# Kernel optimization log

Hardware: AMD Instinct MI355X
Metric: run time of the kernel (lower is better)

## Reference

```python
import jax, jax.numpy as jnp
import numpy as np

BATCH, T, N_STATES, EMIT = 128, 8192, 128, 64


def setup_inputs() -> dict:
    key = jax.random.key(0)
    kobs, kI, kA, kB = jax.random.split(key, 4)
    # one-hot observation sequences, as fed to the RNN cell
    obs = jax.random.randint(kobs, (BATCH, T), 0, EMIT)
    inputs = jax.nn.one_hot(obs, EMIT, dtype=jnp.float32)  # [B, T, EMIT]
    # valid probability parameters (model.I/A/B produce normalized matrices)
    I = jax.nn.softmax(jax.random.normal(kI, (N_STATES,), dtype=jnp.float32))
    A = jax.nn.softmax(jax.random.normal(kA, (N_STATES, N_STATES), dtype=jnp.float32), axis=-1)
    B = jax.nn.softmax(jax.random.normal(kB, (EMIT, N_STATES), dtype=jnp.float32), axis=0)
    return {"inputs": inputs, "I": I, "A": A, "B": B}


def reference(inputs, I, A, B):
    # HMM scaled forward algorithm, exactly the CgpHmmCell.call math,
    # run over the sequence with lax.scan (what keras.layers.RNN does step-wise).
    x = jnp.swapaxes(inputs, 0, 1)  # [T, batch, EMIT]

    # t == 0 (count == 1): R = I, Z = 1
    E0 = x[0] @ B                               # [batch, S]
    alpha0 = E0 * I[None, :]                    # [batch, S]
    loglik0 = jnp.log(jnp.sum(alpha0, axis=-1, keepdims=True))  # [batch, 1]

    def step(carry, x_t):
        alpha, loglik = carry
        Z = jnp.sum(alpha, axis=-1, keepdims=True)      # Z_{i-1}
        R = (alpha / Z) @ A                             # scaled forward @ A
        E = x_t @ B                                     # emission probs
        alpha_new = E * R
        loglik_new = loglik + jnp.log(jnp.sum(alpha_new, axis=-1, keepdims=True))
        return (alpha_new, loglik_new), None

    (alpha_f, loglik_f), _ = jax.lax.scan(step, (alpha0, loglik0), x[1:])
    return alpha_f, loglik_f
```

## Files before the change

kernel.cpp:

```cpp
#include <hip/hip_runtime.h>


#define BATCH 128
#define TLEN 8192
#define NS 128
#define EMIT 64
#define NCHUNK 256
#define CLEN (TLEN / NCHUNK)
#define WARM 8
#define BG 8
#define BSTR 132
#define LN64 4.158883083359672f

typedef __attribute__((ext_vector_type(8))) short short8;
typedef __attribute__((ext_vector_type(4))) float floatx4;
typedef __attribute__((ext_vector_type(4))) unsigned int uintx4;

__device__ __forceinline__ unsigned f2bf(float f) {
    return (__float_as_uint(f) + 0x8000u) >> 16;
}

__global__ __launch_bounds__(256) void decode_onehot(
        const floatx4* __restrict__ x, unsigned char* __restrict__ obsG,
        float* __restrict__ out_ll) {
    if (blockIdx.x == 0 && threadIdx.x < BATCH) out_ll[threadIdx.x] = 0.f;
    int base = blockIdx.x * 512 + threadIdx.x;
    #pragma unroll
    for (int h = 0; h < 2; ++h) {
        int i = base + h * 256;
        floatx4 v = __builtin_nontemporal_load(&x[i]);
        float s = v.x + v.y + v.z + v.w;
        if (s > 0.5f) {
            int e = (v.y > 0.5f) ? 1 : (v.z > 0.5f) ? 2 : (v.w > 0.5f) ? 3 : 0;
            int elem = (i << 2) + e;
            int row = elem >> 6;
            int col = elem & 63;
            int b = row >> 13;
            int t = row & (TLEN - 1);
            obsG[(b >> 4) * (16 * TLEN) + (b & 15) * TLEN + t] = (unsigned char)col;
        }
    }
}

__global__ __launch_bounds__(64) void hmm_scan(
        const float* __restrict__ Amat,
        const float* __restrict__ Bmat,
        const float* __restrict__ Ivec,
        const unsigned char* __restrict__ obsG,
        float* __restrict__ out_alpha,
        float* __restrict__ out_ll)
{
    __shared__ unsigned short Bl[EMIT * BSTR];

    const int lane = threadIdx.x;
    const int n = lane & 15;
    const int q = lane >> 4;
    const int bg = blockIdx.x >> 8;
    const int c = blockIdx.x & (NCHUNK - 1);
    const bool first = (c == 0);
    const bool lastc = (c == NCHUNK - 1);
    const int steps = first ? CLEN : (CLEN + WARM);
    const int t0 = first ? 0 : c * CLEN - WARM;

    for (int i = lane; i < EMIT * NS; i += 64) {
        int e = i >> 7, col = i & (NS - 1);
        Bl[e * BSTR + col] = (unsigned short)f2bf(64.0f * Bmat[i]);
    }

    const unsigned char* orow = obsG + bg * (16 * TLEN) + n * TLEN;
    unsigned ow[10];
    if (first) {
        uintx4 a = *(const uintx4*)(orow);
        uintx4 b = *(const uintx4*)(orow + 16);
        ow[0] = a.x; ow[1] = a.y; ow[2] = a.z; ow[3] = a.w;
        ow[4] = b.x; ow[5] = b.y; ow[6] = b.z; ow[7] = b.w;
        ow[8] = 0; ow[9] = 0;
    } else {
        uint2 a = *(const uint2*)(orow + t0);
        uintx4 b = *(const uintx4*)(orow + t0 + 8);
        uintx4 d = *(const uintx4*)(orow + t0 + 24);
        ow[0] = a.x; ow[1] = a.y;
        ow[2] = b.x; ow[3] = b.y; ow[4] = b.z; ow[5] = b.w;
        ow[6] = d.x; ow[7] = d.y; ow[8] = d.z; ow[9] = d.w;
    }

    short8 af[8][4];
    #pragma unroll
    for (int mt = 0; mt < 8; ++mt)
        #pragma unroll
        for (int kf = 0; kf < 4; ++kf) {
            short8 v;
            #pragma unroll
            for (int j = 0; j < 8; ++j) {
                int u = 32 * kf + 8 * q + j;
                int sk = 32 * (u >> 5) + 16 * ((u >> 2) & 1)
                       + 4 * ((u >> 3) & 3) + (u & 3);
                v[j] = (short)f2bf(Amat[sk * NS + 16 * mt + n]);
            }
            af[mt][kf] = v;
        }
    __syncthreads();

    unsigned pk[16];
    #pragma unroll
    for (int i = 0; i < 16; ++i) pk[i] = 0x3C003C00u;

    float s_pre = 1.0f, s_penult = 1.0f, s_end = 1.0f;

    for (int it = 0; it < steps; ++it) {
        floatx4 acc[8];
        if (first && it == 0) {
            #pragma unroll
            for (int mt = 0; mt < 8; ++mt)
                acc[mt] = *(const floatx4*)(Ivec + 16 * mt + 4 * q);
        } else {
            short8 bf[4];
            #pragma unroll
            for (int kf = 0; kf < 4; ++kf) {
                uintx4 u4 = {pk[4 * kf], pk[4 * kf + 1], pk[4 * kf + 2], pk[4 * kf + 3]};
                bf[kf] = __builtin_bit_cast(short8, u4);
            }
            #pragma unroll
            for (int mt = 0; mt < 8; ++mt) {
                floatx4 a = {0.f, 0.f, 0.f, 0.f};
                #pragma unroll
                for (int kf = 0; kf < 4; ++kf)
                    a = __builtin_amdgcn_mfma_f32_16x16x32_bf16(af[mt][kf], bf[kf], a, 0, 0, 0);
                acc[mt] = a;
            }
        }

        int o = (ow[it >> 2] >> ((it & 3) * 8)) & 0xFF;
        int eb = o * BSTR;
        #pragma unroll
        for (int mt = 0; mt < 8; ++mt) {
            const unsigned* ep = (const unsigned*)(Bl + eb + 16 * mt + 4 * q);
            unsigned d0 = ep[0], d1 = ep[1];
            acc[mt].x *= __uint_as_float(d0 << 16);
            acc[mt].y *= __uint_as_float(d0 & 0xFFFF0000u);
            acc[mt].z *= __uint_as_float(d1 << 16);
            acc[mt].w *= __uint_as_float(d1 & 0xFFFF0000u);
        }

        bool need_red = (it == steps - 1) || (!first && it == WARM - 1) ||
                        (lastc && it == steps - 2);
        if (need_red) {
            float zz = 0.f;
            #pragma unroll
            for (int mt = 0; mt < 8; ++mt)
                zz += (acc[mt].x + acc[mt].y) + (acc[mt].z + acc[mt].w);
            zz += __shfl_xor(zz, 16, 64);
            zz += __shfl_xor(zz, 32, 64);
            if (it == steps - 1) s_end = zz;
            else if (lastc && it == steps - 2) s_penult = zz;
            else s_pre = zz;
        }

        if (lastc && it == steps - 1) {
            float inv = 1.0f / (64.0f * s_penult);
            #pragma unroll
            for (int mt = 0; mt < 8; ++mt) {
                floatx4 o4;
                o4.x = acc[mt].x * inv; o4.y = acc[mt].y * inv;
                o4.z = acc[mt].z * inv; o4.w = acc[mt].w * inv;
                *(floatx4*)(out_alpha + (bg * 16 + n) * NS + 16 * mt + 4 * q) = o4;
            }
        }

        #pragma unroll
        for (int mt = 0; mt < 8; ++mt) {
            unsigned u0 = __float_as_uint(acc[mt].x) + 0x8000u;
            unsigned u1 = __float_as_uint(acc[mt].y) + 0x8000u;
            unsigned u2 = __float_as_uint(acc[mt].z) + 0x8000u;
            unsigned u3 = __float_as_uint(acc[mt].w) + 0x8000u;
            pk[2 * mt]     = __builtin_amdgcn_perm(u1, u0, 0x07060302u);
            pk[2 * mt + 1] = __builtin_amdgcn_perm(u3, u2, 0x07060302u);
        }
    }

    if (q == 0) {
        float ll = __logf(s_end) - __logf(s_pre) - (float)CLEN * LN64;
        atomicAdd(&out_ll[bg * 16 + n], ll);
    }
}

extern "C" void kernel_launch(void* const* d_in, const int* in_sizes, int n_in,
                              void* d_out, int out_size, void* d_ws, size_t ws_size,
                              hipStream_t stream) {
    const float* x = (const float*)d_in[0];
    const float* I = (const float*)d_in[1];
    const float* A = (const float*)d_in[2];
    const float* B = (const float*)d_in[3];
    float* out = (float*)d_out;

    unsigned char* obsG = (unsigned char*)d_ws;

    decode_onehot<<<(BATCH * TLEN * 16) / 512, 256, 0, stream>>>(
        (const floatx4*)x, obsG, out + BATCH * NS);
    hmm_scan<<<BG * NCHUNK, 64, 0, stream>>>(A, B, I, obsG, out, out + BATCH * NS);
}
```

Before: 388.8 us.

## Fuse one-hot decoding into the HMM scan kernel with pipelined prefetch

Removes the separate decode kernel and its byte-index workspace. The scan kernel now streams the one-hot input rows itself, issuing nontemporal loads two steps ahead and decoding each step's observations through a small double-buffered LDS array while the MFMA recurrence runs. It also raises wave priority around the MFMA block, adds an occupancy hint to the launch bounds, and zeroes the log-likelihood output with a memset. The aim is to hide the one-hot input traffic behind the latency-bound serial recurrence. The risks are that the warm-up overlap makes each block re-read part of the input and that each step now waits on more memory latency.

```diff
diff --git a/kernel.cpp b/kernel.cpp
--- a/kernel.cpp
+++ b/kernel.cpp
@@ -20,37 +20,116 @@
     return (__float_as_uint(f) + 0x8000u) >> 16;
 }
 
-__global__ __launch_bounds__(256) void decode_onehot(
-        const floatx4* __restrict__ x, unsigned char* __restrict__ obsG,
-        float* __restrict__ out_ll) {
-    if (blockIdx.x == 0 && threadIdx.x < BATCH) out_ll[threadIdx.x] = 0.f;
-    int base = blockIdx.x * 512 + threadIdx.x;
-    #pragma unroll
-    for (int h = 0; h < 2; ++h) {
-        int i = base + h * 256;
-        floatx4 v = __builtin_nontemporal_load(&x[i]);
-        float s = v.x + v.y + v.z + v.w;
-        if (s > 0.5f) {
-            int e = (v.y > 0.5f) ? 1 : (v.z > 0.5f) ? 2 : (v.w > 0.5f) ? 3 : 0;
-            int elem = (i << 2) + e;
-            int row = elem >> 6;
-            int col = elem & 63;
-            int b = row >> 13;
-            int t = row & (TLEN - 1);
-            obsG[(b >> 4) * (16 * TLEN) + (b & 15) * TLEN + t] = (unsigned char)col;
-        }
-    }
-}
-
-__global__ __launch_bounds__(64) void hmm_scan(
+
+#define ISSUE(P0, P1, P2, P3, s) do {                                     \
+    int _o = (s) * 16;                                                    \
+    P0 = __builtin_nontemporal_load(&X[b0 + _o]);                         \
+    P1 = __builtin_nontemporal_load(&X[b1 + _o]);                         \
+    P2 = __builtin_nontemporal_load(&X[b2 + _o]);                         \
+    P3 = __builtin_nontemporal_load(&X[b3 + _o]);                         \
+} while (0)
+
+#define DEC1(V, g, par) do {                                              \
+    float _s = V.x + V.y + V.z + V.w;                                     \
+    if (_s > 0.5f) {                                                      \
+        int _e = (dcol << 2) +                                            \
+                 ((V.y > 0.5f) ? 1 : (V.z > 0.5f) ? 2 :                   \
+                  (V.w > 0.5f) ? 3 : 0);                                  \
+        obsb[par][4 * (g) + drow] = (unsigned char)_e;                    \
+    }                                                                     \
+} while (0)
+
+#define DECODE(P0, P1, P2, P3, par, dst) do {                             \
+    DEC1(P0, 0, par); DEC1(P1, 1, par);                                   \
+    DEC1(P2, 2, par); DEC1(P3, 3, par);                                   \
+    dst = obsb[par][n];                                                   \
+} while (0)
+
+#define STEP(IT, RA0, RA1, RA2, RA3, RB0, RB1, RB2, RB3, PAR) do {        \
+    int _nx = (IT) + 2; if (_nx > steps - 1) _nx = steps - 1;             \
+    ISSUE(RA0, RA1, RA2, RA3, _nx);                                       \
+    int _onx = o_cur;                                                     \
+    if ((IT) + 1 < steps) DECODE(RB0, RB1, RB2, RB3, PAR, _onx);          \
+    floatx4 acc[8];                                                       \
+    if (first && (IT) == 0) {                                             \
+        _Pragma("unroll")                                                 \
+        for (int mt = 0; mt < 8; ++mt)                                    \
+            acc[mt] = *(const floatx4*)(Ivec + 16 * mt + 4 * q);          \
+    } else {                                                              \
+        short8 bf[4];                                                     \
+        _Pragma("unroll")                                                 \
+        for (int kf = 0; kf < 4; ++kf) {                                  \
+            uintx4 _u4 = {pk[4 * kf], pk[4 * kf + 1],                     \
+                          pk[4 * kf + 2], pk[4 * kf + 3]};                \
+            bf[kf] = __builtin_bit_cast(short8, _u4);                     \
+        }                                                                 \
+        __builtin_amdgcn_s_setprio(1);                                    \
+        _Pragma("unroll")                                                 \
+        for (int mt = 0; mt < 8; ++mt) {                                  \
+            floatx4 _a = {0.f, 0.f, 0.f, 0.f};                            \
+            _Pragma("unroll")                                             \
+            for (int kf = 0; kf < 4; ++kf)                                \
+                _a = __builtin_amdgcn_mfma_f32_16x16x32_bf16(             \
+                        af[mt][kf], bf[kf], _a, 0, 0, 0);                 \
+            acc[mt] = _a;                                                 \
+        }                                                                 \
+        __builtin_amdgcn_s_setprio(0);                                    \
+    }                                                                     \
+    int _eb = o_cur * BSTR;                                               \
+    _Pragma("unroll")                                                     \
+    for (int mt = 0; mt < 8; ++mt) {                                      \
+        const unsigned* _ep = (const unsigned*)(Bl + _eb + 16*mt + 4*q);  \
+        unsigned _d0 = _ep[0], _d1 = _ep[1];                              \
+        acc[mt].x *= __uint_as_float(_d0 << 16);                          \
+        acc[mt].y *= __uint_as_float(_d0 & 0xFFFF0000u);                  \
+        acc[mt].z *= __uint_as_float(_d1 << 16);                          \
+        acc[mt].w *= __uint_as_float(_d1 & 0xFFFF0000u);                  \
+    }                                                                     \
+    bool _red = ((IT) == steps - 1) || (!first && (IT) == WARM - 1) ||    \
+                (lastc && (IT) == steps - 2);                             \
+    if (_red) {                                                           \
+        float _zz = 0.f;                                                  \
+        _Pragma("unroll")                                                 \
+        for (int mt = 0; mt < 8; ++mt)                                    \
+            _zz += (acc[mt].x + acc[mt].y) + (acc[mt].z + acc[mt].w);     \
+        _zz += __shfl_xor(_zz, 16, 64);                                   \
+        _zz += __shfl_xor(_zz, 32, 64);                                   \
+        if ((IT) == steps - 1) s_end = _zz;                               \
+        else if (lastc && (IT) == steps - 2) s_penult = _zz;              \
+        else s_pre = _zz;                                                 \
+    }                                                                     \
+    if (lastc && (IT) == steps - 1) {                                     \
+        float _inv = 1.0f / (64.0f * s_penult);                           \
+        _Pragma("unroll")                                                 \
+        for (int mt = 0; mt < 8; ++mt) {                                  \
+            floatx4 _o4;                                                  \
+            _o4.x = acc[mt].x * _inv; _o4.y = acc[mt].y * _inv;           \
+            _o4.z = acc[mt].z * _inv; _o4.w = acc[mt].w * _inv;           \
+            *(floatx4*)(out_alpha + (bg*16 + n)*NS + 16*mt + 4*q) = _o4;  \
+        }                                                                 \
+    }                                                                     \
+    _Pragma("unroll")                                                     \
+    for (int mt = 0; mt < 8; ++mt) {                                      \
+        unsigned _u0 = __float_as_uint(acc[mt].x) + 0x8000u;              \
+        unsigned _u1 = __float_as_uint(acc[mt].y) + 0x8000u;              \
+        unsigned _u2 = __float_as_uint(acc[mt].z) + 0x8000u;              \
+        unsigned _u3 = __float_as_uint(acc[mt].w) + 0x8000u;              \
+        pk[2*mt]     = __builtin_amdgcn_perm(_u1, _u0, 0x07060302u);      \
+        pk[2*mt + 1] = __builtin_amdgcn_perm(_u3, _u2, 0x07060302u);      \
+    }                                                                     \
+    o_cur = _onx;                                                         \
+} while (0)
+
+__global__ __launch_bounds__(64, 2) void hmm_scan(
         const float* __restrict__ Amat,
         const float* __restrict__ Bmat,
         const float* __restrict__ Ivec,
-        const unsigned char* __restrict__ obsG,
+        const floatx4* __restrict__ X,
         float* __restrict__ out_alpha,
         float* __restrict__ out_ll)
 {
     __shared__ unsigned short Bl[EMIT * BSTR];
+    __shared__ unsigned char obsb[2][16];
 
     const int lane = threadIdx.x;
     const int n = lane & 15;
@@ -65,23 +144,6 @@
     for (int i = lane; i < EMIT * NS; i += 64) {
         int e = i >> 7, col = i & (NS - 1);
         Bl[e * BSTR + col] = (unsigned short)f2bf(64.0f * Bmat[i]);
-    }
-
-    const unsigned char* orow = obsG + bg * (16 * TLEN) + n * TLEN;
-    unsigned ow[10];
-    if (first) {
-        uintx4 a = *(const uintx4*)(orow);
-        uintx4 b = *(const uintx4*)(orow + 16);
-        ow[0] = a.x; ow[1] = a.y; ow[2] = a.z; ow[3] = a.w;
-        ow[4] = b.x; ow[5] = b.y; ow[6] = b.z; ow[7] = b.w;
-        ow[8] = 0; ow[9] = 0;
-    } else {
-        uint2 a = *(const uint2*)(orow + t0);
-        uintx4 b = *(const uintx4*)(orow + t0 + 8);
-        uintx4 d = *(const uintx4*)(orow + t0 + 24);
-        ow[0] = a.x; ow[1] = a.y;
-        ow[2] = b.x; ow[3] = b.y; ow[4] = b.z; ow[5] = b.w;
-        ow[6] = d.x; ow[7] = d.y; ow[8] = d.z; ow[9] = d.w;
     }
 
     short8 af[8][4];
@@ -99,7 +161,19 @@
             }
             af[mt][kf] = v;
         }
-    __syncthreads();
+
+    const int drow = lane >> 4;
+    const int dcol = lane & 15;
+    const int b0 = ((bg * 16 +  0 + drow) * TLEN + t0) * 16 + dcol;
+    const int b1 = ((bg * 16 +  4 + drow) * TLEN + t0) * 16 + dcol;
+    const int b2 = ((bg * 16 +  8 + drow) * TLEN + t0) * 16 + dcol;
+    const int b3 = ((bg * 16 + 12 + drow) * TLEN + t0) * 16 + dcol;
+
+    floatx4 A0, A1, A2, A3, B0, B1, B2, B3;
+    ISSUE(A0, A1, A2, A3, 0);
+    ISSUE(B0, B1, B2, B3, 1);
+    int o_cur;
+    { int _tmp; DECODE(A0, A1, A2, A3, 0, _tmp); o_cur = _tmp; }
 
     unsigned pk[16];
     #pragma unroll
@@ -107,75 +181,11 @@
 
     float s_pre = 1.0f, s_penult = 1.0f, s_end = 1.0f;
 
-    for (int it = 0; it < steps; ++it) {
-        floatx4 acc[8];
-        if (first && it == 0) {
-            #pragma unroll
-            for (int mt = 0; mt < 8; ++mt)
-                acc[mt] = *(const floatx4*)(Ivec + 16 * mt + 4 * q);
-        } else {
-            short8 bf[4];
-            #pragma unroll
-            for (int kf = 0; kf < 4; ++kf) {
-                uintx4 u4 = {pk[4 * kf], pk[4 * kf + 1], pk[4 * kf + 2], pk[4 * kf + 3]};
-                bf[kf] = __builtin_bit_cast(short8, u4);
-            }
-            #pragma unroll
-            for (int mt = 0; mt < 8; ++mt) {
-                floatx4 a = {0.f, 0.f, 0.f, 0.f};
-                #pragma unroll
-                for (int kf = 0; kf < 4; ++kf)
-                    a = __builtin_amdgcn_mfma_f32_16x16x32_bf16(af[mt][kf], bf[kf], a, 0, 0, 0);
-                acc[mt] = a;
-            }
-        }
-
-        int o = (ow[it >> 2] >> ((it & 3) * 8)) & 0xFF;
-        int eb = o * BSTR;
-        #pragma unroll
-        for (int mt = 0; mt < 8; ++mt) {
-            const unsigned* ep = (const unsigned*)(Bl + eb + 16 * mt + 4 * q);
-            unsigned d0 = ep[0], d1 = ep[1];
-            acc[mt].x *= __uint_as_float(d0 << 16);
-            acc[mt].y *= __uint_as_float(d0 & 0xFFFF0000u);
-            acc[mt].z *= __uint_as_float(d1 << 16);
-            acc[mt].w *= __uint_as_float(d1 & 0xFFFF0000u);
-        }
-
-        bool need_red = (it == steps - 1) || (!first && it == WARM - 1) ||
-                        (lastc && it == steps - 2);
-        if (need_red) {
-            float zz = 0.f;
-            #pragma unroll
-            for (int mt = 0; mt < 8; ++mt)
-                zz += (acc[mt].x + acc[mt].y) + (acc[mt].z + acc[mt].w);
-            zz += __shfl_xor(zz, 16, 64);
-            zz += __shfl_xor(zz, 32, 64);
-            if (it == steps - 1) s_end = zz;
-            else if (lastc && it == steps - 2) s_penult = zz;
-            else s_pre = zz;
-        }
-
-        if (lastc && it == steps - 1) {
-            float inv = 1.0f / (64.0f * s_penult);
-            #pragma unroll
-            for (int mt = 0; mt < 8; ++mt) {
-                floatx4 o4;
-                o4.x = acc[mt].x * inv; o4.y = acc[mt].y * inv;
-                o4.z = acc[mt].z * inv; o4.w = acc[mt].w * inv;
-                *(floatx4*)(out_alpha + (bg * 16 + n) * NS + 16 * mt + 4 * q) = o4;
-            }
-        }
-
-        #pragma unroll
-        for (int mt = 0; mt < 8; ++mt) {
-            unsigned u0 = __float_as_uint(acc[mt].x) + 0x8000u;
-            unsigned u1 = __float_as_uint(acc[mt].y) + 0x8000u;
-            unsigned u2 = __float_as_uint(acc[mt].z) + 0x8000u;
-            unsigned u3 = __float_as_uint(acc[mt].w) + 0x8000u;
-            pk[2 * mt]     = __builtin_amdgcn_perm(u1, u0, 0x07060302u);
-            pk[2 * mt + 1] = __builtin_amdgcn_perm(u3, u2, 0x07060302u);
-        }
+    __syncthreads();
+
+    for (int it = 0; it < steps; it += 2) {
+        STEP(it,     A0, A1, A2, A3, B0, B1, B2, B3, 1);
+        STEP(it + 1, B0, B1, B2, B3, A0, A1, A2, A3, 0);
     }
 
     if (q == 0) {
@@ -193,9 +203,8 @@
     const float* B = (const float*)d_in[3];
     float* out = (float*)d_out;
 
-    unsigned char* obsG = (unsigned char*)d_ws;
-
-    decode_onehot<<<(BATCH * TLEN * 16) / 512, 256, 0, stream>>>(
-        (const floatx4*)x, obsG, out + BATCH * NS);
-    hmm_scan<<<BG * NCHUNK, 64, 0, stream>>>(A, B, I, obsG, out, out + BATCH * NS);
+    hipMemsetAsync(out + BATCH * NS, 0, BATCH * sizeof(float), stream);
+
+    hmm_scan<<<BG * NCHUNK, 64, 0, stream>>>(
+        A, B, I, (const floatx4*)x, out, out + BATCH * NS);
 }
```

After: 406.5 us. 1.05x slower.
